# Kernel tuning notes

Measured on AMD Instinct MI355X. Metric: run time of the kernel, lower is better.

The kernel has to match this reference:

```python
import jax, jax.numpy as jnp
import numpy as np


def setup_inputs() -> dict:
    key = jax.random.key(0)
    k1, k2, k3, k4, k5 = jax.random.split(key, 5)
    B, H, W, C = 4, 64, 64, 512
    x = jax.random.normal(k1, (B, H, W, C), dtype=jnp.float32)
    # 1x1 conv kernels (no bias), he_normal-ish scaling
    W1 = jax.random.normal(k2, (C, C // 8), dtype=jnp.float32) * (2.0 / C) ** 0.5
    W2 = jax.random.normal(k3, (C, C // 8), dtype=jnp.float32) * (2.0 / C) ** 0.5
    W3 = jax.random.normal(k4, (C, C), dtype=jnp.float32) * (2.0 / C) ** 0.5
    gamma = jax.random.normal(k5, (1,), dtype=jnp.float32) * 0.1
    return {"x": x, "W1": W1, "W2": W2, "W3": W3, "gamma": gamma}


def reference(x, W1, W2, W3, gamma):
    B, H, W, C = x.shape
    HW = H * W
    Cr = C // 8
    # 1x1 convs == per-position channel projections
    b = jnp.einsum('bhwc,cd->bhwd', x, W1).reshape(B, HW, Cr)   # queries
    c = jnp.einsum('bhwc,cd->bhwd', x, W2).reshape(B, HW, Cr)   # keys
    d = jnp.einsum('bhwc,cd->bhwd', x, W3).reshape(B, HW, C)    # values
    # bc[b,i,j] = <b_i, c_j>  (no 1/sqrt(d) scaling, per original)
    bc = jnp.einsum('bik,bjk->bij', b, c)                        # [B, HW, HW]
    sm = jax.nn.softmax(bc, axis=-1)
    # keras dot(axes=[1,2]): contract HW axis of d with last axis of sm -> [B, C, HW]
    bcd = jnp.einsum('bjc,bij->bci', d, sm)                      # [B, C, HW]
    # original applies a raw Reshape (NOT a transpose) to (h, w, C) — faithful
    bcd = bcd.reshape(B, H, W, C)
    return gamma * bcd + x
```

## Files before the change

kernel.cpp:

```cpp
#include <hip/hip_runtime.h>
#include <hip/hip_bf16.h>
#include <stdint.h>

typedef __bf16 bf16x8 __attribute__((ext_vector_type(8)));
typedef unsigned short ushort8 __attribute__((ext_vector_type(8)));
typedef unsigned short ushort4v __attribute__((ext_vector_type(4)));
typedef float f32x4 __attribute__((ext_vector_type(4)));
typedef unsigned int uint32x2 __attribute__((ext_vector_type(2)));
typedef unsigned int uint32x4 __attribute__((ext_vector_type(4)));

#define MFMA16(a, b, c) __builtin_amdgcn_mfma_f32_16x16x32_bf16((a), (b), (c), 0, 0, 0)

__device__ __forceinline__ unsigned short f2bf(float f) {
    uint32_t u = __float_as_uint(f);
    u += 0x7FFFu + ((u >> 16) & 1u);
    return (unsigned short)(u >> 16);
}
__device__ __forceinline__ float bf2f(unsigned short u) {
    return __uint_as_float(((uint32_t)u) << 16);
}
__device__ __forceinline__ uint32_t pk_bf16(float lo, float hi) {
    uint32_t r;
    asm("v_cvt_pk_bf16_f32 %0, %1, %2" : "=v"(r) : "v"(lo), "v"(hi));
    return r;
}

__global__ void k_build_wt(const float* __restrict__ W1, const float* __restrict__ W2,
                           const float* __restrict__ W3, unsigned short* __restrict__ Wt) {
    int idx = blockIdx.x * 256 + threadIdx.x;
    int n = idx >> 9;
    int k = idx & 511;
    float v;
    if (n < 64)       v = W1[k * 64 + n];
    else if (n < 128) v = W2[k * 64 + (n - 64)];
    else              v = W3[k * 512 + (n - 128)];
    Wt[idx] = f2bf(v);
}

__global__ __launch_bounds__(512, 2) void k_proj(const float* __restrict__ x,
                                                 const unsigned short* __restrict__ Wt,
                                                 unsigned short* __restrict__ Qb,
                                                 unsigned short* __restrict__ Kb,
                                                 unsigned short* __restrict__ Vt) {
    __shared__ __align__(16) unsigned short As[64 * 520];
    const int tid  = threadIdx.x;
    const int lane = tid & 63;
    const int w    = tid >> 6;
    const int m0   = blockIdx.x * 64;
    const int col  = lane & 15, quad = lane >> 4;

#pragma unroll
    for (int itr = 0; itr < 16; ++itr) {
        int idx = itr * 512 + tid;
        int row = idx >> 7, c4 = (idx & 127) << 2;
        f32x4 v = *(const f32x4*)(x + (m0 + row) * 512 + c4);
        uint32x2 o;
        o[0] = pk_bf16(v[0], v[1]); o[1] = pk_bf16(v[2], v[3]);
        *(uint32x2*)(&As[row * 520 + c4]) = o;
    }
    __syncthreads();

    f32x4 acc[4][5] = {};
    bf16x8 bcur[5], bnxt[5];
    const unsigned short* bp = Wt + quad * 8;
#pragma unroll
    for (int nt = 0; nt < 5; ++nt)
        bcur[nt] = *(const bf16x8*)(bp + (w * 80 + nt * 16 + col) * 512);

    for (int k = 0; k < 16; ++k) {
        int kn = (k + 1) & 15;
#pragma unroll
        for (int nt = 0; nt < 5; ++nt)
            bnxt[nt] = *(const bf16x8*)(bp + (w * 80 + nt * 16 + col) * 512 + kn * 32);
        bf16x8 af[4];
#pragma unroll
        for (int it = 0; it < 4; ++it)
            af[it] = *(const bf16x8*)(&As[(it * 16 + col) * 520 + k * 32 + quad * 8]);
#pragma unroll
        for (int it = 0; it < 4; ++it)
#pragma unroll
            for (int nt = 0; nt < 5; ++nt)
                acc[it][nt] = MFMA16(af[it], bcur[nt], acc[it][nt]);
#pragma unroll
        for (int nt = 0; nt < 5; ++nt) bcur[nt] = bnxt[nt];
    }

#pragma unroll
    for (int nt = 0; nt < 5; ++nt) {
        int n0 = w * 80 + nt * 16;
        if (n0 < 128) {
            unsigned short* dst = (n0 < 64) ? Qb : Kb;
            int nc = (n0 < 64) ? (n0 + col) : (n0 - 64 + col);
#pragma unroll
            for (int it = 0; it < 4; ++it) {
                int ig = m0 + it * 16 + quad * 4;
#pragma unroll
                for (int r = 0; r < 4; ++r)
                    dst[(ig + r) * 64 + nc] = f2bf(acc[it][nt][r]);
            }
        } else {
            int vrow = n0 - 128 + col;
#pragma unroll
            for (int it = 0; it < 4; ++it) {
                int ig = m0 + it * 16 + quad * 4;
                int b = ig >> 12, ii = ig & 4095;
                uint32x2 pk;
                pk[0] = pk_bf16(acc[it][nt][0], acc[it][nt][1]);
                pk[1] = pk_bf16(acc[it][nt][2], acc[it][nt][3]);
                *(uint32x2*)(Vt + ((b * 512 + vrow) << 12) + ii) = pk;
            }
        }
    }
}

__global__ __launch_bounds__(512, 2) void k_flash(const unsigned short* __restrict__ Qb,
                                                  const unsigned short* __restrict__ Kb,
                                                  const unsigned short* __restrict__ Vt,
                                                  unsigned short* __restrict__ Op,
                                                  float* __restrict__ ml) {
    __shared__ __align__(16) unsigned short Qs[128 * 72];
    __shared__ __align__(16) float          Ss[128 * 132];
    __shared__ __align__(16) unsigned short Ps[128 * 136];
    __shared__ float m_s[128], l_s[128], al_s[128];

    const int tid  = threadIdx.x;
    const int lane = tid & 63;
    const int w    = tid >> 6;
    const int col  = lane & 15, quad = lane >> 4;
    const int xcd  = blockIdx.x & 7;
    const int b    = xcd >> 1;
    const int jh   = xcd & 1;
    const int i0   = (blockIdx.x >> 3) * 128;

    const unsigned short* Qbase = Qb + (b * 4096 + i0) * 64;
    const unsigned short* Kbase = Kb + b * 4096 * 64;
    const unsigned short* Vbase = Vt + b * 512 * 4096;

    if (tid < 128) { m_s[tid] = -3.0e38f; l_s[tid] = 0.0f; }
    {
#pragma unroll
        for (int half = 0; half < 2; ++half) {
            int row = half * 64 + (tid >> 3), ch = tid & 7;
            *(ushort8*)(&Qs[row * 72 + ch * 8]) =
                *(const ushort8*)(Qbase + row * 64 + ch * 8);
        }
    }
    __syncthreads();

    f32x4 acc[8][4] = {};

    for (int jj = 0; jj < 16; ++jj) {
        const int j0 = jh * 2048 + jj * 128;
        {
            const unsigned short* kp = Kbase + (j0 + w * 16 + col) * 64 + quad * 8;
            bf16x8 kf0 = *(const bf16x8*)(kp);
            bf16x8 kf1 = *(const bf16x8*)(kp + 32);
#pragma unroll
            for (int it = 0; it < 8; ++it) {
                bf16x8 q0 = *(const bf16x8*)(&Qs[(it * 16 + col) * 72 + quad * 8]);
                bf16x8 q1 = *(const bf16x8*)(&Qs[(it * 16 + col) * 72 + 32 + quad * 8]);
                f32x4 s = {};
                s = MFMA16(q0, kf0, s);
                s = MFMA16(q1, kf1, s);
                int rb = it * 16 + quad * 4;
#pragma unroll
                for (int r = 0; r < 4; ++r) Ss[(rb + r) * 132 + w * 16 + col] = s[r];
            }
        }
        bf16x8 vf0[4][2];
#pragma unroll
        for (int ct = 0; ct < 4; ++ct) {
            const unsigned short* vp = Vbase + (w * 64 + ct * 16 + col) * 4096 + j0 + quad * 8;
            vf0[ct][0] = *(const bf16x8*)(vp);
            vf0[ct][1] = *(const bf16x8*)(vp + 32);
        }
        __syncthreads();
        {
            int row = tid >> 2, g = tid & 3;
            float* spA = &Ss[row * 132 + g * 16];
            float* spB = &Ss[row * 132 + (g + 4) * 16];
            f32x4 v0 = *(f32x4*)(spA + 0);
            f32x4 v1 = *(f32x4*)(spA + 4);
            f32x4 v2 = *(f32x4*)(spA + 8);
            f32x4 v3 = *(f32x4*)(spA + 12);
            f32x4 u0 = *(f32x4*)(spB + 0);
            f32x4 u1 = *(f32x4*)(spB + 4);
            f32x4 u2 = *(f32x4*)(spB + 8);
            f32x4 u3 = *(f32x4*)(spB + 12);
            float mx = fmaxf(fmaxf(fmaxf(v0[0], v0[1]), fmaxf(v0[2], v0[3])),
                             fmaxf(fmaxf(v1[0], v1[1]), fmaxf(v1[2], v1[3])));
            mx = fmaxf(mx, fmaxf(fmaxf(fmaxf(v2[0], v2[1]), fmaxf(v2[2], v2[3])),
                                 fmaxf(fmaxf(v3[0], v3[1]), fmaxf(v3[2], v3[3]))));
            mx = fmaxf(mx, fmaxf(fmaxf(fmaxf(u0[0], u0[1]), fmaxf(u0[2], u0[3])),
                                 fmaxf(fmaxf(u1[0], u1[1]), fmaxf(u1[2], u1[3]))));
            mx = fmaxf(mx, fmaxf(fmaxf(fmaxf(u2[0], u2[1]), fmaxf(u2[2], u2[3])),
                                 fmaxf(fmaxf(u3[0], u3[1]), fmaxf(u3[2], u3[3]))));
            mx = fmaxf(mx, __shfl_xor(mx, 1, 4));
            mx = fmaxf(mx, __shfl_xor(mx, 2, 4));
            float mo = m_s[row];
            float mn = fmaxf(mo, mx);
            float al = __expf(mo - mn);
#pragma unroll
            for (int i = 0; i < 4; ++i) {
                v0[i] = __expf(v0[i] - mn); v1[i] = __expf(v1[i] - mn);
                v2[i] = __expf(v2[i] - mn); v3[i] = __expf(v3[i] - mn);
                u0[i] = __expf(u0[i] - mn); u1[i] = __expf(u1[i] - mn);
                u2[i] = __expf(u2[i] - mn); u3[i] = __expf(u3[i] - mn);
            }
            float sum = (v0[0]+v0[1]+v0[2]+v0[3]) + (v1[0]+v1[1]+v1[2]+v1[3])
                      + (v2[0]+v2[1]+v2[2]+v2[3]) + (v3[0]+v3[1]+v3[2]+v3[3])
                      + (u0[0]+u0[1]+u0[2]+u0[3]) + (u1[0]+u1[1]+u1[2]+u1[3])
                      + (u2[0]+u2[1]+u2[2]+u2[3]) + (u3[0]+u3[1]+u3[2]+u3[3]);
            uint32x4 w0, w1;
            w0[0] = pk_bf16(v0[0], v0[1]); w0[1] = pk_bf16(v0[2], v0[3]);
            w0[2] = pk_bf16(v1[0], v1[1]); w0[3] = pk_bf16(v1[2], v1[3]);
            w1[0] = pk_bf16(v2[0], v2[1]); w1[1] = pk_bf16(v2[2], v2[3]);
            w1[2] = pk_bf16(v3[0], v3[1]); w1[3] = pk_bf16(v3[2], v3[3]);
            *(uint32x4*)(&Ps[row * 136 + g * 16])     = w0;
            *(uint32x4*)(&Ps[row * 136 + g * 16 + 8]) = w1;
            uint32x4 w2, w3;
            w2[0] = pk_bf16(u0[0], u0[1]); w2[1] = pk_bf16(u0[2], u0[3]);
            w2[2] = pk_bf16(u1[0], u1[1]); w2[3] = pk_bf16(u1[2], u1[3]);
            w3[0] = pk_bf16(u2[0], u2[1]); w3[1] = pk_bf16(u2[2], u2[3]);
            w3[2] = pk_bf16(u3[0], u3[1]); w3[3] = pk_bf16(u3[2], u3[3]);
            *(uint32x4*)(&Ps[row * 136 + (g + 4) * 16])     = w2;
            *(uint32x4*)(&Ps[row * 136 + (g + 4) * 16 + 8]) = w3;
            sum += __shfl_xor(sum, 1, 4);
            sum += __shfl_xor(sum, 2, 4);
            if (g == 0) { m_s[row] = mn; l_s[row] = al * l_s[row] + sum; al_s[row] = al; }
        }
        __syncthreads();
#pragma unroll
        for (int it = 0; it < 8; ++it) {
            int rb = it * 16 + quad * 4;
            f32x4 av;
            av[0] = al_s[rb]; av[1] = al_s[rb + 1]; av[2] = al_s[rb + 2]; av[3] = al_s[rb + 3];
#pragma unroll
            for (int ct = 0; ct < 4; ++ct) acc[it][ct] *= av;
        }
        __builtin_amdgcn_s_setprio(1);
#pragma unroll
        for (int it = 0; it < 8; ++it) {
            bf16x8 pf0 = *(const bf16x8*)(&Ps[(it * 16 + col) * 136 + quad * 8]);
            bf16x8 pf1 = *(const bf16x8*)(&Ps[(it * 16 + col) * 136 + 32 + quad * 8]);
#pragma unroll
            for (int ct = 0; ct < 4; ++ct) {
                acc[it][ct] = MFMA16(pf0, vf0[ct][0], acc[it][ct]);
                acc[it][ct] = MFMA16(pf1, vf0[ct][1], acc[it][ct]);
            }
        }
        __builtin_amdgcn_s_setprio(0);
        bf16x8 vf1[4][2];
#pragma unroll
        for (int ct = 0; ct < 4; ++ct) {
            const unsigned short* vp = Vbase + (w * 64 + ct * 16 + col) * 4096 + j0 + quad * 8;
            vf1[ct][0] = *(const bf16x8*)(vp + 64);
            vf1[ct][1] = *(const bf16x8*)(vp + 96);
        }
        __builtin_amdgcn_s_setprio(1);
#pragma unroll
        for (int it = 0; it < 8; ++it) {
            bf16x8 pf2 = *(const bf16x8*)(&Ps[(it * 16 + col) * 136 + 64 + quad * 8]);
            bf16x8 pf3 = *(const bf16x8*)(&Ps[(it * 16 + col) * 136 + 96 + quad * 8]);
#pragma unroll
            for (int ct = 0; ct < 4; ++ct) {
                acc[it][ct] = MFMA16(pf2, vf1[ct][0], acc[it][ct]);
                acc[it][ct] = MFMA16(pf3, vf1[ct][1], acc[it][ct]);
            }
        }
        __builtin_amdgcn_s_setprio(0);
    }

    unsigned short* obh = Op + jh * 8388608 + b * 2097152;
#pragma unroll
    for (int it = 0; it < 8; ++it) {
        int rb = it * 16 + quad * 4;
#pragma unroll
        for (int ct = 0; ct < 4; ++ct) {
            int cg = w * 64 + ct * 16 + col;
            int f = cg * 4096 + i0 + rb;
            uint32x2 pk;
            f32x4 a = acc[it][ct];
            pk[0] = pk_bf16(a[0], a[1]); pk[1] = pk_bf16(a[2], a[3]);
            *(uint32x2*)(obh + f) = pk;
        }
    }
    if (tid < 128) {
        float2 v; v.x = m_s[tid]; v.y = l_s[tid];
        ((float2*)ml)[(jh * 4 + b) * 4096 + i0 + tid] = v;
    }
}

__global__ void k_mlw(const float* __restrict__ ml, const float* __restrict__ gamma,
                      float* __restrict__ cw) {
    int t = blockIdx.x * 256 + threadIdx.x;
    float2 a = ((const float2*)ml)[t];
    float2 c = ((const float2*)ml)[16384 + t];
    float M = fmaxf(a.x, c.x);
    float e0 = __expf(a.x - M), e1 = __expf(c.x - M);
    float g = gamma[0] / (e0 * a.y + e1 * c.y);
    float2 o; o.x = g * e0; o.y = g * e1;
    ((float2*)cw)[t] = o;
}

__global__ void k_combine(const unsigned short* __restrict__ Op,
                          const float* __restrict__ cw,
                          const float* __restrict__ x, float* __restrict__ out) {
    int t = blockIdx.x * 256 + threadIdx.x;
    int f = t << 2;
    int b = f >> 21, i = f & 4095;
    const float* cwf = cw + (((b << 12) + i) << 1);
    f32x4 wa = *(const f32x4*)(cwf);
    f32x4 wb = *(const f32x4*)(cwf + 4);
    ushort4v o0 = *(const ushort4v*)(Op + f);
    ushort4v o1 = *(const ushort4v*)(Op + 8388608 + f);
    f32x4 xv = *(const f32x4*)(x + f);
    f32x4 o;
    o[0] = wa[0] * bf2f(o0[0]) + wa[1] * bf2f(o1[0]) + xv[0];
    o[1] = wa[2] * bf2f(o0[1]) + wa[3] * bf2f(o1[1]) + xv[1];
    o[2] = wb[0] * bf2f(o0[2]) + wb[1] * bf2f(o1[2]) + xv[2];
    o[3] = wb[2] * bf2f(o0[3]) + wb[3] * bf2f(o1[3]) + xv[3];
    *(f32x4*)(out + f) = o;
}

extern "C" void kernel_launch(void* const* d_in, const int* in_sizes, int n_in,
                              void* d_out, int out_size, void* d_ws, size_t ws_size,
                              hipStream_t stream) {
    const float* x  = (const float*)d_in[0];
    const float* W1 = (const float*)d_in[1];
    const float* W2 = (const float*)d_in[2];
    const float* W3 = (const float*)d_in[3];
    const float* gm = (const float*)d_in[4];
    float* out = (float*)d_out;

    char* ws = (char*)d_ws;
    unsigned short* Wt = (unsigned short*)(ws);
    unsigned short* Qb = (unsigned short*)(ws + (1u  << 20));
    unsigned short* Kb = (unsigned short*)(ws + (3u  << 20));
    unsigned short* Vt = (unsigned short*)(ws + (5u  << 20));
    unsigned short* Op = (unsigned short*)(ws + (21u << 20));
    float*          ml = (float*)        (ws + (53u << 20));
    float*          cw = (float*)        (ws + (53u << 20) + 262144);

    hipLaunchKernelGGL(k_build_wt, dim3(1280), dim3(256), 0, stream, W1, W2, W3, Wt);
    hipLaunchKernelGGL(k_proj,     dim3(256),  dim3(512), 0, stream, x, Wt, Qb, Kb, Vt);
    hipLaunchKernelGGL(k_flash,    dim3(256),  dim3(512), 0, stream, Qb, Kb, Vt, Op, ml);
    hipLaunchKernelGGL(k_mlw,      dim3(64),   dim3(256), 0, stream, ml, gm, cw);
    hipLaunchKernelGGL(k_combine,  dim3(8192), dim3(256), 0, stream, Op, cw, x, out);
}
```

Measured before the change: 221.7 us.

## Switch flash attention MFMA tiles from 16x16x32 to 32x32x16 bf16

Rewrites the QK^T and PV matrix products in the flash kernel to use 32x32x16 MFMA instructions instead of 16x16x32, remapping lane-to-row/column indexing, the score-tile partition across waves, the accumulator layout, the alpha rescale and the output store. The larger tiles give more reuse per operand fetched into registers and need fewer LDS reads of P per MFMA. The second-half V loads are also moved earlier, ahead of the first PV MFMA block, to overlap global latency with compute. The cost is more register pressure from the larger accumulators and V fragments, plus different LDS store patterns for S.

```diff
diff --git a/kernel.cpp b/kernel.cpp
--- a/kernel.cpp
+++ b/kernel.cpp
@@ -6,10 +6,12 @@
 typedef unsigned short ushort8 __attribute__((ext_vector_type(8)));
 typedef unsigned short ushort4v __attribute__((ext_vector_type(4)));
 typedef float f32x4 __attribute__((ext_vector_type(4)));
+typedef float f32x16 __attribute__((ext_vector_type(16)));
 typedef unsigned int uint32x2 __attribute__((ext_vector_type(2)));
 typedef unsigned int uint32x4 __attribute__((ext_vector_type(4)));
 
 #define MFMA16(a, b, c) __builtin_amdgcn_mfma_f32_16x16x32_bf16((a), (b), (c), 0, 0, 0)
+#define MFMA32(a, b, c) __builtin_amdgcn_mfma_f32_32x32x16_bf16((a), (b), (c), 0, 0, 0)
 
 __device__ __forceinline__ unsigned short f2bf(float f) {
     uint32_t u = __float_as_uint(f);
@@ -126,7 +128,9 @@
     const int tid  = threadIdx.x;
     const int lane = tid & 63;
     const int w    = tid >> 6;
-    const int col  = lane & 15, quad = lane >> 4;
+    const int l31  = lane & 31, l5 = lane >> 5;
+    const int kt   = w & 3;
+    const int rh   = w >> 2;
     const int xcd  = blockIdx.x & 7;
     const int b    = xcd >> 1;
     const int jh   = xcd & 1;
@@ -147,33 +151,38 @@
     }
     __syncthreads();
 
-    f32x4 acc[8][4] = {};
+    f32x16 acc[4][2] = {};
 
     for (int jj = 0; jj < 16; ++jj) {
         const int j0 = jh * 2048 + jj * 128;
         {
-            const unsigned short* kp = Kbase + (j0 + w * 16 + col) * 64 + quad * 8;
-            bf16x8 kf0 = *(const bf16x8*)(kp);
-            bf16x8 kf1 = *(const bf16x8*)(kp + 32);
-#pragma unroll
-            for (int it = 0; it < 8; ++it) {
-                bf16x8 q0 = *(const bf16x8*)(&Qs[(it * 16 + col) * 72 + quad * 8]);
-                bf16x8 q1 = *(const bf16x8*)(&Qs[(it * 16 + col) * 72 + 32 + quad * 8]);
-                f32x4 s = {};
-                s = MFMA16(q0, kf0, s);
-                s = MFMA16(q1, kf1, s);
-                int rb = it * 16 + quad * 4;
-#pragma unroll
-                for (int r = 0; r < 4; ++r) Ss[(rb + r) * 132 + w * 16 + col] = s[r];
-            }
-        }
-        bf16x8 vf0[4][2];
-#pragma unroll
-        for (int ct = 0; ct < 4; ++ct) {
-            const unsigned short* vp = Vbase + (w * 64 + ct * 16 + col) * 4096 + j0 + quad * 8;
-            vf0[ct][0] = *(const bf16x8*)(vp);
-            vf0[ct][1] = *(const bf16x8*)(vp + 32);
-        }
+            bf16x8 kB[4];
+            const unsigned short* kp = Kbase + (j0 + kt * 32 + l31) * 64 + l5 * 8;
+#pragma unroll
+            for (int ks = 0; ks < 4; ++ks)
+                kB[ks] = *(const bf16x8*)(kp + ks * 16);
+#pragma unroll
+            for (int rtl = 0; rtl < 2; ++rtl) {
+                int rowA = (rh * 2 + rtl) * 32 + l31;
+                f32x16 s = {};
+#pragma unroll
+                for (int ks = 0; ks < 4; ++ks) {
+                    bf16x8 qA = *(const bf16x8*)(&Qs[rowA * 72 + ks * 16 + l5 * 8]);
+                    s = MFMA32(qA, kB[ks], s);
+                }
+                int rbase = (rh * 2 + rtl) * 32 + 4 * l5;
+#pragma unroll
+                for (int r = 0; r < 16; ++r)
+                    Ss[(rbase + (r & 3) + 8 * (r >> 2)) * 132 + kt * 32 + l31] = s[r];
+            }
+        }
+        const unsigned short* vpb = Vbase + (w * 64 + l31) * 4096 + j0 + l5 * 8;
+        bf16x8 vf0[2][4];
+#pragma unroll
+        for (int ct = 0; ct < 2; ++ct)
+#pragma unroll
+            for (int ks = 0; ks < 4; ++ks)
+                vf0[ct][ks] = *(const bf16x8*)(vpb + ct * 32 * 4096 + ks * 16);
         __syncthreads();
         {
             int row = tid >> 2, g = tid & 3;
@@ -231,60 +240,61 @@
         }
         __syncthreads();
 #pragma unroll
-        for (int it = 0; it < 8; ++it) {
-            int rb = it * 16 + quad * 4;
-            f32x4 av;
-            av[0] = al_s[rb]; av[1] = al_s[rb + 1]; av[2] = al_s[rb + 2]; av[3] = al_s[rb + 3];
-#pragma unroll
-            for (int ct = 0; ct < 4; ++ct) acc[it][ct] *= av;
-        }
+        for (int rt = 0; rt < 4; ++rt)
+#pragma unroll
+            for (int q = 0; q < 4; ++q) {
+                int rb = rt * 32 + 8 * q + 4 * l5;
+                f32x4 av = *(const f32x4*)(&al_s[rb]);
+#pragma unroll
+                for (int ct = 0; ct < 2; ++ct)
+#pragma unroll
+                    for (int e = 0; e < 4; ++e)
+                        acc[rt][ct][q * 4 + e] *= av[e];
+            }
+        bf16x8 vf1[2][4];
+#pragma unroll
+        for (int ct = 0; ct < 2; ++ct)
+#pragma unroll
+            for (int ks = 0; ks < 4; ++ks)
+                vf1[ct][ks] = *(const bf16x8*)(vpb + ct * 32 * 4096 + 64 + ks * 16);
         __builtin_amdgcn_s_setprio(1);
 #pragma unroll
-        for (int it = 0; it < 8; ++it) {
-            bf16x8 pf0 = *(const bf16x8*)(&Ps[(it * 16 + col) * 136 + quad * 8]);
-            bf16x8 pf1 = *(const bf16x8*)(&Ps[(it * 16 + col) * 136 + 32 + quad * 8]);
-#pragma unroll
-            for (int ct = 0; ct < 4; ++ct) {
-                acc[it][ct] = MFMA16(pf0, vf0[ct][0], acc[it][ct]);
-                acc[it][ct] = MFMA16(pf1, vf0[ct][1], acc[it][ct]);
-            }
-        }
+        for (int rt = 0; rt < 4; ++rt)
+#pragma unroll
+            for (int ks = 0; ks < 4; ++ks) {
+                bf16x8 pf = *(const bf16x8*)(&Ps[(rt * 32 + l31) * 136 + ks * 16 + l5 * 8]);
+                acc[rt][0] = MFMA32(pf, vf0[0][ks], acc[rt][0]);
+                acc[rt][1] = MFMA32(pf, vf0[1][ks], acc[rt][1]);
+            }
         __builtin_amdgcn_s_setprio(0);
-        bf16x8 vf1[4][2];
-#pragma unroll
-        for (int ct = 0; ct < 4; ++ct) {
-            const unsigned short* vp = Vbase + (w * 64 + ct * 16 + col) * 4096 + j0 + quad * 8;
-            vf1[ct][0] = *(const bf16x8*)(vp + 64);
-            vf1[ct][1] = *(const bf16x8*)(vp + 96);
-        }
         __builtin_amdgcn_s_setprio(1);
 #pragma unroll
-        for (int it = 0; it < 8; ++it) {
-            bf16x8 pf2 = *(const bf16x8*)(&Ps[(it * 16 + col) * 136 + 64 + quad * 8]);
-            bf16x8 pf3 = *(const bf16x8*)(&Ps[(it * 16 + col) * 136 + 96 + quad * 8]);
-#pragma unroll
-            for (int ct = 0; ct < 4; ++ct) {
-                acc[it][ct] = MFMA16(pf2, vf1[ct][0], acc[it][ct]);
-                acc[it][ct] = MFMA16(pf3, vf1[ct][1], acc[it][ct]);
-            }
-        }
+        for (int rt = 0; rt < 4; ++rt)
+#pragma unroll
+            for (int ks = 0; ks < 4; ++ks) {
+                bf16x8 pf = *(const bf16x8*)(&Ps[(rt * 32 + l31) * 136 + 64 + ks * 16 + l5 * 8]);
+                acc[rt][0] = MFMA32(pf, vf1[0][ks], acc[rt][0]);
+                acc[rt][1] = MFMA32(pf, vf1[1][ks], acc[rt][1]);
+            }
         __builtin_amdgcn_s_setprio(0);
     }
 
     unsigned short* obh = Op + jh * 8388608 + b * 2097152;
 #pragma unroll
-    for (int it = 0; it < 8; ++it) {
-        int rb = it * 16 + quad * 4;
-#pragma unroll
-        for (int ct = 0; ct < 4; ++ct) {
-            int cg = w * 64 + ct * 16 + col;
-            int f = cg * 4096 + i0 + rb;
-            uint32x2 pk;
-            f32x4 a = acc[it][ct];
-            pk[0] = pk_bf16(a[0], a[1]); pk[1] = pk_bf16(a[2], a[3]);
-            *(uint32x2*)(obh + f) = pk;
-        }
-    }
+    for (int rt = 0; rt < 4; ++rt)
+#pragma unroll
+        for (int ct = 0; ct < 2; ++ct) {
+            int cg = w * 64 + ct * 32 + l31;
+#pragma unroll
+            for (int q = 0; q < 4; ++q) {
+                int rowb = rt * 32 + 8 * q + 4 * l5;
+                int f = cg * 4096 + i0 + rowb;
+                uint32x2 pk;
+                pk[0] = pk_bf16(acc[rt][ct][q * 4 + 0], acc[rt][ct][q * 4 + 1]);
+                pk[1] = pk_bf16(acc[rt][ct][q * 4 + 2], acc[rt][ct][q * 4 + 3]);
+                *(uint32x2*)(obh + f) = pk;
+            }
+        }
     if (tid < 128) {
         float2 v; v.x = m_s[tid]; v.y = l_s[tid];
         ((float2*)ml)[(jh * 4 + b) * 4096 + i0 + tid] = v;
```

Measured after the change: 224.1 us. Within noise of the previous version (+1.1%).
